# Kernel optimization log

Hardware: AMD Instinct MI355X
Metric: run time of the kernel (lower is better)

Reference implementation:

```python
import jax, jax.numpy as jnp
import numpy as np
from jax import lax

K = 11  # AvgPool kernel
PAD = 5
EPS = 1e-5


def _box_avg(x):
    # Separable 11x11 box filter, stride 1, zero padding (count_include_pad=True)
    # x: [B, C, H, W]
    s = lax.reduce_window(x, 0.0, lax.add, (1, 1, K, 1), (1, 1, 1, 1),
                          [(0, 0), (0, 0), (PAD, PAD), (0, 0)])
    s = lax.reduce_window(s, 0.0, lax.add, (1, 1, 1, K), (1, 1, 1, 1),
                          [(0, 0), (0, 0), (0, 0), (PAD, PAD)])
    return s * (1.0 / (K * K))


def _bn(x, g, b, m, v):
    # eval-mode BatchNorm2d over channel dim (axis 1)
    scale = (g / jnp.sqrt(v + EPS))[None, :, None, None]
    shift = (b - m * g / jnp.sqrt(v + EPS))[None, :, None, None]
    return x * scale + shift


def setup_inputs() -> dict:
    key = jax.random.key(0)
    ks = jax.random.split(key, 13)
    B, C, H, W = 16, 256, 128, 128
    Ch = C // 2
    return {
        "x": jax.random.normal(ks[0], (B, C, H, W), jnp.float32),
        "w1": jax.random.normal(ks[1], (Ch, C), jnp.float32) * (1.0 / np.sqrt(C)),
        "b1": jax.random.normal(ks[2], (Ch,), jnp.float32) * 0.1,
        "bn1_g": jax.random.uniform(ks[3], (Ch,), jnp.float32, 0.5, 1.5),
        "bn1_b": jax.random.normal(ks[4], (Ch,), jnp.float32) * 0.1,
        "bn1_m": jax.random.normal(ks[5], (Ch,), jnp.float32) * 0.1,
        "bn1_v": jax.random.uniform(ks[6], (Ch,), jnp.float32, 0.5, 1.5),
        "w2": jax.random.normal(ks[7], (C, Ch), jnp.float32) * (1.0 / np.sqrt(Ch)),
        "b2": jax.random.normal(ks[8], (C,), jnp.float32) * 0.1,
        "bn2_g": jax.random.uniform(ks[9], (C,), jnp.float32, 0.5, 1.5),
        "bn2_b": jax.random.normal(ks[10], (C,), jnp.float32) * 0.1,
        "bn2_m": jax.random.normal(ks[11], (C,), jnp.float32) * 0.1,
        "bn2_v": jax.random.uniform(ks[12], (C,), jnp.float32, 0.5, 1.5),
    }


def reference(x, w1, b1, bn1_g, bn1_b, bn1_m, bn1_v,
              w2, b2, bn2_g, bn2_b, bn2_m, bn2_v):
    # edge features: high-pass via box-filter subtraction
    edge = x - _box_avg(x)
    # 1x1 conv -> BN -> ReLU
    h = jnp.einsum('bchw,oc->bohw', edge, w1) + b1[None, :, None, None]
    h = jax.nn.relu(_bn(h, bn1_g, bn1_b, bn1_m, bn1_v))
    # 1x1 conv -> BN -> Sigmoid
    w = jnp.einsum('bchw,oc->bohw', h, w2) + b2[None, :, None, None]
    w = jax.nn.sigmoid(_bn(w, bn2_g, bn2_b, bn2_m, bn2_v))
    # gated residual enhancement
    return w * x + x
```

## Files before the change

### kernel.cpp

```cpp
#include <hip/hip_runtime.h>

#define BB 16
#define CC 256
#define CH 128
#define HH 128
#define WW 128
#define HW (HH*WW)
#define KPOOL 11
#define PADP 5
#define EPS 1e-5f

typedef __attribute__((ext_vector_type(8))) short s16x8;
typedef __attribute__((ext_vector_type(4))) float f32x4;
typedef __attribute__((ext_vector_type(8))) unsigned short u16x8;
typedef __attribute__((ext_vector_type(4))) unsigned short u16x4;
typedef __attribute__((ext_vector_type(4))) unsigned int u32x4;

static __device__ __forceinline__ unsigned short f2bf(float f) {
    unsigned int u = __float_as_uint(f);
    u = u + 0x7fffu + ((u >> 16) & 1u);
    return (unsigned short)(u >> 16);
}
static __device__ __forceinline__ float bf2f(unsigned short h) {
    return __uint_as_float(((unsigned int)h) << 16);
}

#define MFMA16(a, b, c) __builtin_amdgcn_mfma_f32_16x16x32_bf16((a), (b), (c), 0, 0, 0)

__global__ __launch_bounds__(256) void prep_kernel(
    const float* __restrict__ w1, const float* __restrict__ b1,
    const float* __restrict__ g1, const float* __restrict__ be1,
    const float* __restrict__ m1, const float* __restrict__ v1,
    const float* __restrict__ w2, const float* __restrict__ b2,
    const float* __restrict__ g2, const float* __restrict__ be2,
    const float* __restrict__ m2, const float* __restrict__ v2,
    unsigned short* __restrict__ w1h, unsigned short* __restrict__ w1l,
    unsigned short* __restrict__ w2h, unsigned short* __restrict__ w2l,
    float* __restrict__ A1, float* __restrict__ B1,
    float* __restrict__ A2, float* __restrict__ B2)
{
    int i = blockIdx.x * 256 + threadIdx.x;
    if (i < CH * CC) {
        float w = w1[i];
        unsigned short hi = f2bf(w);
        w1h[i] = hi;
        w1l[i] = f2bf(w - bf2f(hi));
        float u = w2[i];
        unsigned short hi2 = f2bf(u);
        w2h[i] = hi2;
        w2l[i] = f2bf(u - bf2f(hi2));
    }
    if (i < CH) {
        float sc = g1[i] * rsqrtf(v1[i] + EPS);
        A1[i] = sc;
        B1[i] = be1[i] + (b1[i] - m1[i]) * sc;
    }
    if (i < CC) {
        float sc = g2[i] * rsqrtf(v2[i] + EPS);
        A2[i] = sc;
        B2[i] = be2[i] + (b2[i] - m2[i]) * sc;
    }
}

__global__ __launch_bounds__(256) void box_edge_kernel(
    const float* __restrict__ x, unsigned short* __restrict__ edge)
{
    constexpr int RB = 16;
    int blk  = blockIdx.x;
    int band = blk & 7;
    int bc   = blk >> 3;
    const float* img = x + (size_t)bc * HW;

    __shared__ float tile[RB + 2*PADP][WW];
    __shared__ float vs[RB][WW];

    int h0 = band * RB;

    for (int idx = threadIdx.x; idx < (RB + 2*PADP) * (WW/4); idx += blockDim.x) {
        int r  = idx >> 5;
        int w4 = idx & 31;
        int h  = h0 - PADP + r;
        f32x4 v = {0.f, 0.f, 0.f, 0.f};
        if (h >= 0 && h < HH) v = *(const f32x4*)(img + h * WW + w4 * 4);
        *(f32x4*)&tile[r][w4 * 4] = v;
    }
    __syncthreads();

    for (int idx = threadIdx.x; idx < RB * WW; idx += blockDim.x) {
        int r = idx >> 7;
        int w = idx & 127;
        float s = 0.f;
#pragma unroll
        for (int j = 0; j < KPOOL; ++j) s += tile[r + j][w];
        vs[r][w] = s;
    }
    __syncthreads();

    for (int idx = threadIdx.x; idx < RB * WW; idx += blockDim.x) {
        int r = idx >> 7;
        int w = idx & 127;
        float s = 0.f;
#pragma unroll
        for (int dx = -PADP; dx <= PADP; ++dx) {
            int ww = w + dx;
            if (ww >= 0 && ww < WW) s += vs[r][ww];
        }
        float e = tile[r + PADP][w] - s * (1.f / (KPOOL * KPOOL));
        edge[(size_t)bc * HW + (size_t)(h0 + r) * WW + w] = f2bf(e);
    }
}

__global__ __launch_bounds__(256) void transpose_kernel(
    const unsigned short* __restrict__ edge_raw, unsigned short* __restrict__ edge_t)
{
    int blk = blockIdx.x;
    int c0 = (blk & 3) * 64;
    int p0 = ((blk >> 2) & 255) * 64;
    int b  = blk >> 10;

    __shared__ unsigned int lds32[64 * 33];

    int t  = threadIdx.x;
    int rp = t >> 3;
    int sl = t & 7;

    size_t rowA = ((size_t)(b * CC + c0 + 2 * rp)) << 14;
    u16x8 a = *(const u16x8*)(edge_raw + rowA + p0 + sl * 8);
    u16x8 c = *(const u16x8*)(edge_raw + rowA + (1 << 14) + p0 + sl * 8);

#pragma unroll
    for (int j = 0; j < 8; ++j) {
        unsigned int w = (unsigned int)a[j] | ((unsigned int)c[j] << 16);
        lds32[(sl * 8 + j) * 33 + rp] = w;
    }
    __syncthreads();

    int p = t >> 2;
    int q = t & 3;
    u32x4 o0, o1;
#pragma unroll
    for (int k = 0; k < 4; ++k) o0[k] = lds32[p * 33 + q * 8 + k];
#pragma unroll
    for (int k = 0; k < 4; ++k) o1[k] = lds32[p * 33 + q * 8 + 4 + k];

    unsigned short* dst = edge_t + (((size_t)(b * HW + p0 + p)) << 8) + c0 + q * 16;
    *(u32x4*)dst       = o0;
    *(u32x4*)(dst + 8) = o1;
}

__global__ __launch_bounds__(512, 6) void gemm12_fused(
    const unsigned short* __restrict__ edge_t,
    const unsigned short* __restrict__ w1h, const unsigned short* __restrict__ w1l,
    const float* __restrict__ A1, const float* __restrict__ B1,
    const unsigned short* __restrict__ w2h, const unsigned short* __restrict__ w2l,
    const float* __restrict__ A2, const float* __restrict__ B2,
    const float* __restrict__ x, float* __restrict__ out)
{
    const int blk  = blockIdx.x;
    const int b    = blk >> 8;
    const int p0   = (blk & 255) * 64;
    const int tid  = threadIdx.x;
    const int lane = tid & 63;
    const int l15  = lane & 15;
    const int l4   = lane >> 4;
    const int wv   = tid >> 6;

    __shared__ unsigned short eT[64 * 256];
    __shared__ unsigned short hT[64 * 128];

    const unsigned short* E = edge_t + (((size_t)(b * HW + p0)) << 8);

#pragma unroll
    for (int i = 0; i < 4; ++i) {
        int L  = i * 512 + tid;
        int pl = L >> 5;
        int s  = L & 31;
        int g  = s ^ (pl & 7);
        *(u16x8*)&eT[pl * 256 + s * 8] = *(const u16x8*)(E + pl * 256 + g * 8);
    }
    __syncthreads();

    const f32x4 z4 = {0.f, 0.f, 0.f, 0.f};

    {
        const int o = wv * 16 + l15;
        f32x4 acc[4];
#pragma unroll
        for (int fp = 0; fp < 4; ++fp) acc[fp] = z4;

#pragma unroll
        for (int ks = 0; ks < 8; ++ks) {
            s16x8 bfr[4];
#pragma unroll
            for (int fp = 0; fp < 4; ++fp) {
                int pl = fp * 16 + l15;
                bfr[fp] = *(const s16x8*)&eT[pl * 256 + ((ks * 4 + l4) ^ (pl & 7)) * 8];
            }
            size_t wo = (size_t)o * CC + ks * 32 + l4 * 8;
            s16x8 ah = *(const s16x8*)(w1h + wo);
            s16x8 al = *(const s16x8*)(w1l + wo);
#pragma unroll
            for (int fp = 0; fp < 4; ++fp) {
                acc[fp] = MFMA16(ah, bfr[fp], acc[fp]);
                acc[fp] = MFMA16(al, bfr[fp], acc[fp]);
            }
        }

        int ob = wv * 16 + l4 * 4;
        f32x4 sc = *(const f32x4*)(A1 + ob);
        f32x4 sh = *(const f32x4*)(B1 + ob);
#pragma unroll
        for (int fp = 0; fp < 4; ++fp) {
            int pl = fp * 16 + l15;
            u16x4 hv;
#pragma unroll
            for (int r = 0; r < 4; ++r) {
                float v = acc[fp][r] * sc[r] + sh[r];
                v = fmaxf(v, 0.f);
                hv[r] = f2bf(v);
            }
            *(u16x4*)&hT[pl * 128 + ((ob >> 3) ^ (pl & 7)) * 8 + (ob & 7)] = hv;
        }
    }
    __syncthreads();

    {
        const int o0 = wv * 32;
        f32x4 acc[2][4];
#pragma unroll
        for (int fo = 0; fo < 2; ++fo)
#pragma unroll
            for (int fp = 0; fp < 4; ++fp) acc[fo][fp] = z4;

#pragma unroll
        for (int ks = 0; ks < 4; ++ks) {
            s16x8 bfr[4];
#pragma unroll
            for (int fp = 0; fp < 4; ++fp) {
                int pl = fp * 16 + l15;
                bfr[fp] = *(const s16x8*)&hT[pl * 128 + ((ks * 4 + l4) ^ (pl & 7)) * 8];
            }
#pragma unroll
            for (int fo = 0; fo < 2; ++fo) {
                int o = o0 + fo * 16 + l15;
                size_t wo = (size_t)o * CH + ks * 32 + l4 * 8;
                s16x8 ah = *(const s16x8*)(w2h + wo);
                s16x8 al = *(const s16x8*)(w2l + wo);
#pragma unroll
                for (int fp = 0; fp < 4; ++fp) {
                    acc[fo][fp] = MFMA16(ah, bfr[fp], acc[fo][fp]);
                    acc[fo][fp] = MFMA16(al, bfr[fp], acc[fo][fp]);
                }
            }
        }

#pragma unroll
        for (int fo = 0; fo < 2; ++fo) {
            int ob = o0 + fo * 16 + l4 * 4;
            f32x4 sc = *(const f32x4*)(A2 + ob);
            f32x4 sh = *(const f32x4*)(B2 + ob);
#pragma unroll
            for (int fp = 0; fp < 4; ++fp) {
                int p = p0 + fp * 16 + l15;
#pragma unroll
                for (int r = 0; r < 4; ++r) {
                    float z = acc[fo][fp][r] * sc[r] + sh[r];
                    float gte = 1.f / (1.f + __expf(-z));
                    size_t idx = (((size_t)(b * CC + ob + r)) << 14) + p;
                    out[idx] = x[idx] * (1.f + gte);
                }
            }
        }
    }
}

extern "C" void kernel_launch(void* const* d_in, const int* in_sizes, int n_in,
                              void* d_out, int out_size, void* d_ws, size_t ws_size,
                              hipStream_t stream) {
    const float* x   = (const float*)d_in[0];
    const float* w1  = (const float*)d_in[1];
    const float* b1  = (const float*)d_in[2];
    const float* g1  = (const float*)d_in[3];
    const float* be1 = (const float*)d_in[4];
    const float* m1  = (const float*)d_in[5];
    const float* v1  = (const float*)d_in[6];
    const float* w2  = (const float*)d_in[7];
    const float* b2  = (const float*)d_in[8];
    const float* g2  = (const float*)d_in[9];
    const float* be2 = (const float*)d_in[10];
    const float* m2  = (const float*)d_in[11];
    const float* v2  = (const float*)d_in[12];
    float* out = (float*)d_out;

    const size_t EDGE_BYTES  = (size_t)BB * CC * HW * 2;
    const size_t SMALL_BYTES = 4 * (size_t)CH * CC * 2 + (2 * CH + 2 * CC) * 4;

    unsigned short* edge_raw = (unsigned short*)d_out;
    unsigned short* edge_t;
    char* smalls;
    if (ws_size >= EDGE_BYTES + SMALL_BYTES) {
        edge_t = (unsigned short*)d_ws;
        smalls = (char*)d_ws + EDGE_BYTES;
    } else {
        edge_t = (unsigned short*)((char*)d_out + EDGE_BYTES);
        smalls = (char*)d_ws;
    }
    unsigned short* w1h = (unsigned short*)smalls;
    unsigned short* w1l = w1h + CH * CC;
    unsigned short* w2h = w1l + CH * CC;
    unsigned short* w2l = w2h + CH * CC;
    float* A1v = (float*)(w2l + CH * CC);
    float* B1v = A1v + CH;
    float* A2v = B1v + CH;
    float* B2v = A2v + CC;

    prep_kernel<<<128, 256, 0, stream>>>(w1, b1, g1, be1, m1, v1,
                                         w2, b2, g2, be2, m2, v2,
                                         w1h, w1l, w2h, w2l, A1v, B1v, A2v, B2v);

    box_edge_kernel<<<BB * CC * (HH / 16), 256, 0, stream>>>(x, edge_raw);

    transpose_kernel<<<BB * (HW / 64) * (CC / 64), 256, 0, stream>>>(edge_raw, edge_t);

    gemm12_fused<<<BB * (HW / 64), 512, 0, stream>>>(
        edge_t, w1h, w1l, A1v, B1v, w2h, w2l, A2v, B2v, x, out);
}
```

Baseline: 813.9 us.

## Use sliding-window and prefix-sum box filter; read edge tiles directly from global

The vertical pass of the box filter becomes a running sum over 8 rows per thread, and the horizontal pass becomes a warp-shuffle prefix scan so each output is a difference of two prefix values. This cuts the shared-memory reads per output from 11 to a few. In the fused GEMM kernel, the staging of the edge tile into LDS and its barrier are removed, and the MFMA B fragments are loaded straight from global memory. That frees LDS, which may raise occupancy, but it relies on cache for the reuse across waves and uses less coalesced loads. The prefix-sum subtraction also changes the floating-point rounding slightly.

After: 888.0 us. 1.09x slower.

```diff
diff --git a/kernel.cpp b/kernel.cpp
--- a/kernel.cpp
+++ b/kernel.cpp
@@ -73,10 +73,12 @@
 
     __shared__ float tile[RB + 2*PADP][WW];
     __shared__ float vs[RB][WW];
+    __shared__ float P[RB][WW + 4];
 
     int h0 = band * RB;
-
-    for (int idx = threadIdx.x; idx < (RB + 2*PADP) * (WW/4); idx += blockDim.x) {
+    int t  = threadIdx.x;
+
+    for (int idx = t; idx < (RB + 2*PADP) * (WW/4); idx += 256) {
         int r  = idx >> 5;
         int w4 = idx & 31;
         int h  = h0 - PADP + r;
@@ -86,25 +88,51 @@
     }
     __syncthreads();
 
-    for (int idx = threadIdx.x; idx < RB * WW; idx += blockDim.x) {
-        int r = idx >> 7;
-        int w = idx & 127;
+    {
+        int w = t & 127, half = t >> 7;
+        int r0 = half * 8;
         float s = 0.f;
 #pragma unroll
-        for (int j = 0; j < KPOOL; ++j) s += tile[r + j][w];
-        vs[r][w] = s;
-    }
-    __syncthreads();
-
-    for (int idx = threadIdx.x; idx < RB * WW; idx += blockDim.x) {
-        int r = idx >> 7;
-        int w = idx & 127;
-        float s = 0.f;
-#pragma unroll
-        for (int dx = -PADP; dx <= PADP; ++dx) {
-            int ww = w + dx;
-            if (ww >= 0 && ww < WW) s += vs[r][ww];
-        }
+        for (int j = 0; j < KPOOL; ++j) s += tile[r0 + j][w];
+        vs[r0][w] = s;
+#pragma unroll
+        for (int k = 1; k < 8; ++k) {
+            s += tile[r0 + 10 + k][w] - tile[r0 + k - 1][w];
+            vs[r0 + k][w] = s;
+        }
+    }
+    __syncthreads();
+
+    {
+        int lane = t & 63, wv = t >> 6;
+#pragma unroll
+        for (int rr = 0; rr < 4; ++rr) {
+            int r = wv * 4 + rr;
+            float v = vs[r][lane];
+#pragma unroll
+            for (int d = 1; d < 64; d <<= 1) {
+                float u = __shfl_up(v, d, 64);
+                if (lane >= d) v += u;
+            }
+            P[r][lane + 1] = v;
+            float carry = __shfl(v, 63, 64);
+            float v2 = vs[r][64 + lane];
+#pragma unroll
+            for (int d = 1; d < 64; d <<= 1) {
+                float u = __shfl_up(v2, d, 64);
+                if (lane >= d) v2 += u;
+            }
+            P[r][65 + lane] = v2 + carry;
+            if (lane == 0) P[r][0] = 0.f;
+        }
+    }
+    __syncthreads();
+
+    for (int idx = t; idx < RB * WW; idx += 256) {
+        int r = idx >> 7, w = idx & 127;
+        int a = w - 5; if (a < 0) a = 0;
+        int bq = w + 6; if (bq > 128) bq = 128;
+        float s = P[r][bq] - P[r][a];
         float e = tile[r + PADP][w] - s * (1.f / (KPOOL * KPOOL));
         edge[(size_t)bc * HW + (size_t)(h0 + r) * WW + w] = f2bf(e);
     }
@@ -165,20 +193,9 @@
     const int l4   = lane >> 4;
     const int wv   = tid >> 6;
 
-    __shared__ unsigned short eT[64 * 256];
     __shared__ unsigned short hT[64 * 128];
 
     const unsigned short* E = edge_t + (((size_t)(b * HW + p0)) << 8);
-
-#pragma unroll
-    for (int i = 0; i < 4; ++i) {
-        int L  = i * 512 + tid;
-        int pl = L >> 5;
-        int s  = L & 31;
-        int g  = s ^ (pl & 7);
-        *(u16x8*)&eT[pl * 256 + s * 8] = *(const u16x8*)(E + pl * 256 + g * 8);
-    }
-    __syncthreads();
 
     const f32x4 z4 = {0.f, 0.f, 0.f, 0.f};
 
@@ -194,7 +211,7 @@
 #pragma unroll
             for (int fp = 0; fp < 4; ++fp) {
                 int pl = fp * 16 + l15;
-                bfr[fp] = *(const s16x8*)&eT[pl * 256 + ((ks * 4 + l4) ^ (pl & 7)) * 8];
+                bfr[fp] = *(const s16x8*)(E + ((size_t)pl << 8) + ks * 32 + l4 * 8);
             }
             size_t wo = (size_t)o * CC + ks * 32 + l4 * 8;
             s16x8 ah = *(const s16x8*)(w1h + wo);
```
